# Optimization experiments

Measured on AMD Instinct MI355X. Metric: run time of the kernel, lower is better.

## Reference

```python
import jax, jax.numpy as jnp
import numpy as np

L = 2          # conv layers
N = 50000      # nodes
E = 800000     # edges (before self loops)
F_IN = 256     # raw node features
C = 32         # embed features (out_channels per head)
H = 4          # heads
HC = H * C
ED = 1         # edge feature dim
EPS = 1e-5
NEG_SLOPE = 0.2


def _xavier(k, shape):
    fan_in, fan_out = shape[-2], shape[-1]
    lim = float(np.sqrt(6.0 / (fan_in + fan_out)))
    return jax.random.uniform(k, shape, jnp.float32, -lim, lim)


def setup_inputs() -> dict:
    key = jax.random.key(0)
    ks = jax.random.split(key, 12)
    x = jax.random.normal(ks[0], (N, F_IN), jnp.float32)
    src = jax.random.randint(ks[1], (E,), 0, N, dtype=jnp.int32)
    off = jax.random.randint(ks[2], (E,), 1, N, dtype=jnp.int32)
    dst = (src + off) % N  # guarantees no pre-existing self loops (PyG removes then re-adds them)
    edge_index = jnp.stack([src, dst])
    edge_attr = jax.random.normal(ks[3], (E, ED), jnp.float32)
    return {
        "x": x,
        "edge_index": edge_index,
        "edge_attr": edge_attr,
        "W_emb": _xavier(ks[4], (F_IN, C)),
        "b_emb": jnp.zeros((C,), jnp.float32),
        "ln0_w": jnp.ones((C,), jnp.float32),
        "ln0_b": jnp.zeros((C,), jnp.float32),
        "Wl": _xavier(ks[5], (L, C, HC)),
        "bl": jnp.zeros((L, HC), jnp.float32),
        "Wr": _xavier(ks[6], (L, C, HC)),
        "br": jnp.zeros((L, HC), jnp.float32),
        "We": _xavier(ks[7], (L, ED, HC)),
        "att": jax.random.normal(ks[8], (L, H, C), jnp.float32) * 0.1,
        "gat_b": jnp.zeros((L, HC), jnp.float32),
        "ln1_w": jnp.ones((L, HC), jnp.float32),
        "ln1_b": jnp.zeros((L, HC), jnp.float32),
        "lin_w": _xavier(ks[9], (L, HC, C)),
        "lin_b": jnp.zeros((L, C), jnp.float32),
        "ln2_w": jnp.ones((L, C), jnp.float32),
        "ln2_b": jnp.zeros((L, C), jnp.float32),
    }


def _node_ln(x, w, b):
    # torch.nn.LayerNorm over last dim
    mu = jnp.mean(x, axis=-1, keepdims=True)
    xc = x - mu
    var = jnp.mean(xc * xc, axis=-1, keepdims=True)
    return xc / jnp.sqrt(var + EPS) * w + b


def _graph_ln(x, w, b):
    # torch_geometric.nn.norm.LayerNorm, mode='graph': normalize over ALL nodes+features
    mu = jnp.mean(x)
    xc = x - mu
    var = jnp.mean(xc * xc)
    return xc / jnp.sqrt(var + EPS) * w + b


def _gatv2_layer(h, src, dst, ea, Wl, bl, Wr, br, We, att, gat_b):
    n = h.shape[0]
    xl = (h @ Wl + bl).reshape(n, H, C)   # lin_l(x) -> source transform
    xr = (h @ Wr + br).reshape(n, H, C)   # lin_r(x) -> target transform
    e = (ea @ We).reshape(-1, H, C)       # lin_edge(edge_attr), no bias
    z = jax.nn.leaky_relu(xl[src] + xr[dst] + e, NEG_SLOPE)   # [Etot,H,C]
    logits = jnp.einsum("ehc,hc->eh", z, att)                  # [Etot,H]
    # segment softmax over destination nodes (every node has a self loop)
    m = jax.ops.segment_max(logits, dst, num_segments=n)
    ex = jnp.exp(logits - m[dst])
    s = jax.ops.segment_sum(ex, dst, num_segments=n)
    alpha = ex / s[dst]                                        # [Etot,H]
    msg = alpha[..., None] * xl[src]                           # [Etot,H,C]
    out = jax.ops.segment_sum(msg, dst, num_segments=n)        # [N,H,C]
    return out.reshape(n, HC) + gat_b


def reference(x, edge_index, edge_attr, W_emb, b_emb, ln0_w, ln0_b, Wl, bl, Wr, br,
              We, att, gat_b, ln1_w, ln1_b, lin_w, lin_b, ln2_w, ln2_b):
    n = x.shape[0]
    loop = jnp.arange(n, dtype=edge_index.dtype)
    src = jnp.concatenate([edge_index[0], loop])
    dst = jnp.concatenate([edge_index[1], loop])
    ea = jnp.concatenate([edge_attr, jnp.zeros((n, edge_attr.shape[1]), edge_attr.dtype)])  # fill_value=0.0

    # node_embed: Dropout(eval=identity) -> Linear -> LayerNorm -> ReLU
    h = jax.nn.relu(_node_ln(x @ W_emb + b_emb, ln0_w, ln0_b))
    hs = [h]
    for i in range(L):
        g = _gatv2_layer(h, src, dst, ea, Wl[i], bl[i], Wr[i], br[i], We[i], att[i], gat_b[i])
        g = jax.nn.relu(_graph_ln(g, ln1_w[i], ln1_b[i]))     # PyG graph-mode LayerNorm + ReLU
        g = g @ lin_w[i] + lin_b[i]                            # heads>1 projection back to C
        h = jax.nn.relu(_node_ln(g, ln2_w[i], ln2_b[i]))
        hs.append(h)
    # JumpingKnowledge mode='max': elementwise max over layer outputs
    return jnp.max(jnp.stack(hs, axis=0), axis=0)
```

## Files before the change

### kernel.cpp

```cpp
#include <hip/hip_runtime.h>
#include <hip/hip_fp16.h>

constexpr int kNodes = 50000;
constexpr int kNE    = 800000;
constexpr int kFin   = 256;
constexpr int kC     = 32;
constexpr int kH     = 4;
constexpr int kHC    = 128;
constexpr int kTN    = 16;
constexpr int kWP    = 258;
constexpr int kLWP   = 130;
constexpr int kEmbedBlocks = kNodes / kTN;
constexpr int kHistBlocks  = (kNE + 255) / 256;
constexpr int kTransBlocks = (kNodes + 31) / 32;
constexpr float kEps   = 1e-5f;
constexpr float kSlope = 0.2f;
constexpr float kL2E   = 1.44269504f;
constexpr float kShift2 = 8.0f * 1.44269504f;

template<int CTRL>
__device__ __forceinline__ float dpp_add(float v) {
    int x = __builtin_amdgcn_update_dpp(0, __float_as_int(v), CTRL, 0xF, 0xF, true);
    return v + __int_as_float(x);
}
__device__ __forceinline__ float red16(float p) {
    p = dpp_add<0xB1>(p);
    p = dpp_add<0x4E>(p);
    p = dpp_add<0x141>(p);
    p = dpp_add<0x140>(p);
    return p;
}

__global__ void __launch_bounds__(256) k_fill0(unsigned* __restrict__ p, int n) {
    int i = blockIdx.x * 256 + threadIdx.x;
    if (i < n) p[i] = 0u;
}

__global__ void __launch_bounds__(256) k_embed_hist(
    const float* __restrict__ x, const float* __restrict__ W, const float* __restrict__ b,
    const float* __restrict__ lnw, const float* __restrict__ lnb,
    float* __restrict__ h, float* __restrict__ jk,
    const int* __restrict__ dst, int* __restrict__ deg) {
    __shared__ float sx[kTN * kFin];
    __shared__ float sWt[kC * kWP];
    int t = threadIdx.x;
    if (blockIdx.x >= kEmbedBlocks) {
        int e = (blockIdx.x - kEmbedBlocks) * 256 + t;
        if (e < kNE) atomicAdd(&deg[dst[e]], 1);
        return;
    }
    int n0 = blockIdx.x * kTN;
    for (int i = t; i < kFin * kC; i += 256) {
        int k = i >> 5, c = i & 31;
        sWt[c * kWP + k] = W[i];
    }
    const float* xg = x + (long)n0 * kFin;
    for (int i = t; i < kTN * kFin; i += 256) sx[i] = xg[i];
    __syncthreads();
    int c = t & 31, n2 = t >> 5;
    const float* xa = sx + n2 * kFin;
    const float* xb = sx + (n2 + 8) * kFin;
    const float* wrow = sWt + c * kWP;
    float acc0 = 0.f, acc1 = 0.f;
    #pragma unroll 8
    for (int k = 0; k < kFin; k += 4) {
        float4 x0 = *(const float4*)(xa + k);
        float4 x1 = *(const float4*)(xb + k);
        float2 w0 = *(const float2*)(wrow + k);
        float2 w1 = *(const float2*)(wrow + k + 2);
        acc0 += x0.x * w0.x + x0.y * w0.y + x0.z * w1.x + x0.w * w1.y;
        acc1 += x1.x * w0.x + x1.y * w0.y + x1.z * w1.x + x1.w * w1.y;
    }
    float bc = b[c], lw = lnw[c], lb = lnb[c];
    {
        float y = acc0 + bc;
        float m = y;
        #pragma unroll
        for (int o = 1; o < 32; o <<= 1) m += __shfl_xor(m, o);
        m *= (1.f / kC);
        float xc = y - m, v = xc * xc;
        #pragma unroll
        for (int o = 1; o < 32; o <<= 1) v += __shfl_xor(v, o);
        v *= (1.f / kC);
        float out = fmaxf(xc * rsqrtf(v + kEps) * lw + lb, 0.f);
        int node = n0 + n2;
        h[node * kC + c] = out;
        jk[node * kC + c] = out;
    }
    {
        float y = acc1 + bc;
        float m = y;
        #pragma unroll
        for (int o = 1; o < 32; o <<= 1) m += __shfl_xor(m, o);
        m *= (1.f / kC);
        float xc = y - m, v = xc * xc;
        #pragma unroll
        for (int o = 1; o < 32; o <<= 1) v += __shfl_xor(v, o);
        v *= (1.f / kC);
        float out = fmaxf(xc * rsqrtf(v + kEps) * lw + lb, 0.f);
        int node = n0 + n2 + 8;
        h[node * kC + c] = out;
        jk[node * kC + c] = out;
    }
}

__device__ __forceinline__ void trans_body(
    int bid, float* s_h, const float* __restrict__ h,
    const float* __restrict__ Wl, const float* __restrict__ bl,
    const float* __restrict__ Wr, const float* __restrict__ br,
    __half* __restrict__ xl, float* __restrict__ xr) {
    int t = threadIdx.x;
    int j = t & 127, hf = t >> 7;
    float wl[kC], wr[kC];
    #pragma unroll
    for (int k = 0; k < kC; ++k) { wl[k] = Wl[k * kHC + j]; wr[k] = Wr[k * kHC + j]; }
    float blj = bl[j], brj = br[j];
    int n0 = bid * 32;
    int nn = min(32, kNodes - n0);
    for (int i = t; i < nn * kC; i += 256) s_h[i] = h[n0 * kC + i];
    __syncthreads();
    int nend = min(nn, hf * 16 + 16);
    for (int n = hf * 16; n < nend; ++n) {
        const float4* h4 = (const float4*)(s_h + n * kC);
        float al = blj, ar = brj;
        #pragma unroll
        for (int kq = 0; kq < 8; ++kq) {
            float4 hv = h4[kq];
            al += hv.x * wl[kq*4] + hv.y * wl[kq*4+1] + hv.z * wl[kq*4+2] + hv.w * wl[kq*4+3];
            ar += hv.x * wr[kq*4] + hv.y * wr[kq*4+1] + hv.z * wr[kq*4+2] + hv.w * wr[kq*4+3];
        }
        long g = (long)(n0 + n) * kHC + j;
        xl[g] = __float2half(al);
        xr[g] = ar;
    }
}

__global__ void __launch_bounds__(256) k_trans(
    const float* __restrict__ h,
    const float* __restrict__ Wl, const float* __restrict__ bl,
    const float* __restrict__ Wr, const float* __restrict__ br,
    __half* __restrict__ xl, float* __restrict__ xr) {
    __shared__ float s_h[32 * kC];
    trans_body(blockIdx.x, s_h, h, Wl, bl, Wr, br, xl, xr);
}

__global__ void __launch_bounds__(256) k_trans_reorder(
    const float* __restrict__ h,
    const float* __restrict__ Wl, const float* __restrict__ bl,
    const float* __restrict__ Wr, const float* __restrict__ br,
    __half* __restrict__ xl, float* __restrict__ xr,
    const int* __restrict__ src, const int* __restrict__ dst, const float* __restrict__ ea,
    const int* __restrict__ rowptr, int* __restrict__ cur, int2* __restrict__ epack) {
    __shared__ float s_h[32 * kC];
    if (blockIdx.x < kHistBlocks) {
        int e = blockIdx.x * 256 + threadIdx.x;
        if (e < kNE) {
            int d = dst[e];
            int pos = rowptr[d] + atomicAdd(&cur[d], 1);
            epack[pos] = make_int2(src[e], __float_as_int(ea[e]));
        }
        return;
    }
    trans_body(blockIdx.x - kHistBlocks, s_h, h, Wl, bl, Wr, br, xl, xr);
}

__global__ void __launch_bounds__(256) k_scan1(const int* __restrict__ deg,
                                               int* __restrict__ excl, int* __restrict__ bsum) {
    __shared__ int s[256];
    int t = threadIdx.x;
    int i = blockIdx.x * 256 + t;
    int v = (i < kNodes) ? deg[i] : 0;
    s[t] = v;
    __syncthreads();
    for (int o = 1; o < 256; o <<= 1) {
        int tv = (t >= o) ? s[t - o] : 0;
        __syncthreads();
        s[t] += tv;
        __syncthreads();
    }
    if (i < kNodes) excl[i] = s[t] - v;
    if (t == 255) bsum[blockIdx.x] = s[255];
}

__global__ void __launch_bounds__(256) k_scan2(int* __restrict__ bsum, int nb) {
    __shared__ int s[256];
    int t = threadIdx.x;
    int v = (t < nb) ? bsum[t] : 0;
    s[t] = v;
    __syncthreads();
    for (int o = 1; o < 256; o <<= 1) {
        int tv = (t >= o) ? s[t - o] : 0;
        __syncthreads();
        s[t] += tv;
        __syncthreads();
    }
    if (t < nb) bsum[t] = s[t];
}

__global__ void __launch_bounds__(256) k_scan3(int* __restrict__ excl, const int* __restrict__ bsum) {
    int i = blockIdx.x * 256 + threadIdx.x;
    if (i >= kNodes) return;
    if (blockIdx.x > 0) excl[i] += bsum[blockIdx.x - 1];
}

__global__ void __launch_bounds__(256) k_edge(
    const int* __restrict__ rowptr, const int* __restrict__ deg,
    const int2* __restrict__ epack,
    const __half* __restrict__ xl, float* __restrict__ xrg,
    const float* __restrict__ We, const float* __restrict__ att,
    const float* __restrict__ gat_b, float* __restrict__ ps, float* __restrict__ pq) {
    int t = threadIdx.x & 63;
    int w = __builtin_amdgcn_readfirstlane(threadIdx.x >> 6);
    int d = blockIdx.x * 4 + w;
    const __half2* xl2 = (const __half2*)xl;
    long rowb = (long)d * 64;

    float2 xrv = ((const float2*)xrg)[rowb + t];
    float2 Wev = ((const float2*)We)[t];
    float2 av  = ((const float2*)att)[t];
    av.x *= kL2E; av.y *= kL2E;

    float2 xself = __half22float2(xl2[rowb + t]);

    float z0 = xself.x + xrv.x, z1 = xself.y + xrv.y;
    z0 = fmaxf(z0, kSlope * z0); z1 = fmaxf(z1, kSlope * z1);
    float p = red16(z0 * av.x + z1 * av.y);
    float ee = __builtin_amdgcn_exp2f(p - kShift2);
    float l = ee, o0 = ee * xself.x, o1 = ee * xself.y;

    int base = rowptr[d], cnt = deg[d];
    int e = 0;
    for (; e + 8 <= cnt; e += 8) {
        int se[8]; float ev[8];
        #pragma unroll
        for (int u = 0; u < 8; ++u) {
            int2 ep = epack[base + e + u];
            se[u] = ep.x; ev[u] = __int_as_float(ep.y);
        }
        float2 xv[8]; float pv[8];
        #pragma unroll
        for (int u = 0; u < 8; ++u)
            xv[u] = __half22float2(xl2[(long)se[u] * 64 + t]);
        #pragma unroll
        for (int u = 0; u < 8; ++u) {
            float zz0 = fmaf(ev[u], Wev.x, xrv.x) + xv[u].x;
            float zz1 = fmaf(ev[u], Wev.y, xrv.y) + xv[u].y;
            zz0 = fmaxf(zz0, kSlope * zz0);
            zz1 = fmaxf(zz1, kSlope * zz1);
            pv[u] = red16(zz0 * av.x + zz1 * av.y);
        }
        #pragma unroll
        for (int u = 0; u < 8; ++u) {
            float eeu = __builtin_amdgcn_exp2f(pv[u] - kShift2);
            l += eeu;
            o0 = fmaf(eeu, xv[u].x, o0);
            o1 = fmaf(eeu, xv[u].y, o1);
        }
    }
    for (; e < cnt; ++e) {
        int2 ep = epack[base + e];
        int s = ep.x;
        float eav = __int_as_float(ep.y);
        float2 xv = __half22float2(xl2[(long)s * 64 + t]);
        float zz0 = fmaf(eav, Wev.x, xrv.x) + xv.x;
        float zz1 = fmaf(eav, Wev.y, xrv.y) + xv.y;
        zz0 = fmaxf(zz0, kSlope * zz0);
        zz1 = fmaxf(zz1, kSlope * zz1);
        float pe = red16(zz0 * av.x + zz1 * av.y);
        float eeu = __builtin_amdgcn_exp2f(pe - kShift2);
        l += eeu;
        o0 = fmaf(eeu, xv.x, o0);
        o1 = fmaf(eeu, xv.y, o1);
    }
    float rl = __builtin_amdgcn_rcpf(l);
    float v0 = o0 * rl, v1 = o1 * rl;
    ((float2*)xrg)[rowb + t] = make_float2(v0, v1);
    float2 gb = ((const float2*)gat_b)[t];
    float vb0 = v0 + gb.x, vb1 = v1 + gb.y;
    float s = vb0 + vb1, q = vb0 * vb0 + vb1 * vb1;
    #pragma unroll
    for (int mm = 1; mm < 64; mm <<= 1) { s += __shfl_xor(s, mm); q += __shfl_xor(q, mm); }
    if (t == 0) { ps[d] = s; pq[d] = q; }
}

__global__ void __launch_bounds__(1024) k_statsr(
    const float* __restrict__ ps, const float* __restrict__ pq, float* __restrict__ stats) {
    __shared__ float rs[1024], rq[1024];
    int t = threadIdx.x;
    float s = 0.f, q = 0.f;
    for (int i = t; i < kNodes; i += 1024) { s += ps[i]; q += pq[i]; }
    rs[t] = s; rq[t] = q;
    __syncthreads();
    for (int o = 512; o > 0; o >>= 1) {
        if (t < o) { rs[t] += rs[t + o]; rq[t] += rq[t + o]; }
        __syncthreads();
    }
    if (t == 0) { stats[0] = rs[0]; stats[1] = rq[0]; }
}

__global__ void __launch_bounds__(256) k_post(
    const float* __restrict__ g, const float* __restrict__ gat_b,
    const float* __restrict__ ln1w, const float* __restrict__ ln1b,
    const float* __restrict__ linw, const float* __restrict__ linb,
    const float* __restrict__ ln2w, const float* __restrict__ ln2b,
    const float* __restrict__ stats, const float* __restrict__ jk_in,
    float* __restrict__ h, float* __restrict__ jk_out) {
    __shared__ float s_lwT[kC * kLWP];
    __shared__ float s_vb[8 * kHC];
    int t = threadIdx.x;
    int n0 = blockIdx.x * 8;
    const float inv = 1.f / ((float)kNodes * kHC);
    float mean = stats[0] * inv;
    float var  = stats[1] * inv - mean * mean;
    float rstd = rsqrtf(var + kEps);
    for (int i = t; i < kHC * kC; i += 256) {
        int k = i >> 5, c = i & 31;
        s_lwT[c * kLWP + k] = linw[i];
    }
    for (int i = t; i < 8 * kHC; i += 256) {
        int node = n0 + (i >> 7), f = i & 127;
        float a = (g[(long)node * kHC + f] + gat_b[f] - mean) * rstd * ln1w[f] + ln1b[f];
        s_vb[i] = fmaxf(a, 0.f);
    }
    __syncthreads();
    int n = t >> 5, c = t & 31;
    int node = n0 + n;
    float acc = linb[c];
    const float* vb = s_vb + n * kHC;
    const float* wr = s_lwT + c * kLWP;
    #pragma unroll 8
    for (int k = 0; k < kHC; k += 4) {
        float4 v4 = *(const float4*)(vb + k);
        float2 w0 = *(const float2*)(wr + k);
        float2 w1 = *(const float2*)(wr + k + 2);
        acc += v4.x * w0.x + v4.y * w0.y + v4.z * w1.x + v4.w * w1.y;
    }
    float m = acc;
    #pragma unroll
    for (int mm = 1; mm < 32; mm <<= 1) m += __shfl_xor(m, mm);
    m *= (1.f / kC);
    float dd = acc - m;
    float q = dd * dd;
    #pragma unroll
    for (int mm = 1; mm < 32; mm <<= 1) q += __shfl_xor(q, mm);
    q *= (1.f / kC);
    float out = dd * rsqrtf(q + kEps) * ln2w[c] + ln2b[c];
    out = fmaxf(out, 0.f);
    h[node * kC + c] = out;
    jk_out[node * kC + c] = fmaxf(jk_in[node * kC + c], out);
}

extern "C" void kernel_launch(void* const* d_in, const int* in_sizes, int n_in,
                              void* d_out, int out_size, void* d_ws, size_t ws_size,
                              hipStream_t stream) {
    (void)in_sizes; (void)n_in; (void)out_size; (void)ws_size;
    const float* x     = (const float*)d_in[0];
    const int*   ei    = (const int*)d_in[1];
    const int*   src   = ei;
    const int*   dst   = ei + kNE;
    const float* ea    = (const float*)d_in[2];
    const float* W_emb = (const float*)d_in[3];
    const float* b_emb = (const float*)d_in[4];
    const float* ln0w  = (const float*)d_in[5];
    const float* ln0b  = (const float*)d_in[6];
    const float* Wl    = (const float*)d_in[7];
    const float* bl    = (const float*)d_in[8];
    const float* Wr    = (const float*)d_in[9];
    const float* br    = (const float*)d_in[10];
    const float* We    = (const float*)d_in[11];
    const float* att   = (const float*)d_in[12];
    const float* gat_b = (const float*)d_in[13];
    const float* ln1w  = (const float*)d_in[14];
    const float* ln1b  = (const float*)d_in[15];
    const float* linw  = (const float*)d_in[16];
    const float* linb  = (const float*)d_in[17];
    const float* ln2w  = (const float*)d_in[18];
    const float* ln2b  = (const float*)d_in[19];

    char* wsb = (char*)d_ws;
    float*  h      = (float*)(wsb);
    float*  jk     = (float*)(wsb +  6400000);
    float*  xrg    = (float*)(wsb + 12800000);
    __half* xl     = (__half*)(wsb + 38400000);
    int2*   epack  = (int2*)(wsb + 51200000);
    int*    deg    = (int*)(wsb + 57600000);
    int*    cur    = (int*)(wsb + 57800000);
    int*    rowptr = (int*)(wsb + 58000000);
    int*    bsum   = (int*)(wsb + 58200000);
    float*  stats  = (float*)(wsb + 58201024);
    float*  ps     = (float*)(wsb + 58300000);
    float*  pq     = (float*)(wsb + 58500000);

    const int scanBlocks = (kNodes + 255) / 256;
    const int edgeBlocks = kNodes / 4;
    const int postBlocks = kNodes / 8;

    hipLaunchKernelGGL(k_fill0, dim3((2 * kNodes + 255) / 256), dim3(256), 0, stream,
                       (unsigned*)deg, 2 * kNodes);
    hipLaunchKernelGGL(k_embed_hist, dim3(kEmbedBlocks + kHistBlocks), dim3(256), 0, stream,
                       x, W_emb, b_emb, ln0w, ln0b, h, jk, dst, deg);
    hipLaunchKernelGGL(k_scan1, dim3(scanBlocks), dim3(256), 0, stream, deg, rowptr, bsum);
    hipLaunchKernelGGL(k_scan2, dim3(1), dim3(256), 0, stream, bsum, scanBlocks);
    hipLaunchKernelGGL(k_scan3, dim3(scanBlocks), dim3(256), 0, stream, rowptr, bsum);
    hipLaunchKernelGGL(k_trans_reorder, dim3(kHistBlocks + kTransBlocks), dim3(256), 0, stream,
                       h, Wl, bl, Wr, br, xl, xrg,
                       src, dst, ea, rowptr, cur, epack);
    for (int l = 0; l < 2; ++l) {
        if (l == 1) {
            hipLaunchKernelGGL(k_trans, dim3(kTransBlocks), dim3(256), 0, stream,
                               h, Wl + l * kC * kHC, bl + l * kHC,
                               Wr + l * kC * kHC, br + l * kHC, xl, xrg);
        }
        hipLaunchKernelGGL(k_edge, dim3(edgeBlocks), dim3(256), 0, stream,
                           rowptr, deg, epack, xl, xrg,
                           We + l * kHC, att + l * kH * kC, gat_b + l * kHC, ps, pq);
        hipLaunchKernelGGL(k_statsr, dim3(1), dim3(1024), 0, stream, ps, pq, stats);
        hipLaunchKernelGGL(k_post, dim3(postBlocks), dim3(256), 0, stream,
                           xrg, gat_b + l * kHC, ln1w + l * kHC, ln1b + l * kHC,
                           linw + l * kHC * kC, linb + l * kC,
                           ln2w + l * kC, ln2b + l * kC, stats, jk,
                           h, (l == 1) ? (float*)d_out : jk);
    }
}
```

Before: 463.9 us.

## Process two edges per wavefront in GATv2 edge kernel with half-wave slots

The edge aggregation kernel now splits each 64-lane wavefront into two 32-lane halves. Each half handles alternate edges of the destination node and loads 4 features per lane as an 8-byte half4. The attention dot product uses an 8-lane DPP reduction per head. The two halves' softmax partial sums are merged with a cross-half shuffle at the end. The aim is to double the number of edge gathers in flight per wave and use wider loads. The cost is extra shuffles and more registers per lane.

```diff
diff --git a/kernel.cpp b/kernel.cpp
--- a/kernel.cpp
+++ b/kernel.cpp
@@ -23,11 +23,10 @@
     int x = __builtin_amdgcn_update_dpp(0, __float_as_int(v), CTRL, 0xF, 0xF, true);
     return v + __int_as_float(x);
 }
-__device__ __forceinline__ float red16(float p) {
+__device__ __forceinline__ float red8(float p) {
     p = dpp_add<0xB1>(p);
     p = dpp_add<0x4E>(p);
     p = dpp_add<0x141>(p);
-    p = dpp_add<0x140>(p);
     return p;
 }
 
@@ -209,77 +208,117 @@
     const __half* __restrict__ xl, float* __restrict__ xrg,
     const float* __restrict__ We, const float* __restrict__ att,
     const float* __restrict__ gat_b, float* __restrict__ ps, float* __restrict__ pq) {
+    struct h4 { __half2 a, b; };
     int t = threadIdx.x & 63;
     int w = __builtin_amdgcn_readfirstlane(threadIdx.x >> 6);
     int d = blockIdx.x * 4 + w;
-    const __half2* xl2 = (const __half2*)xl;
-    long rowb = (long)d * 64;
-
-    float2 xrv = ((const float2*)xrg)[rowb + t];
-    float2 Wev = ((const float2*)We)[t];
-    float2 av  = ((const float2*)att)[t];
-    av.x *= kL2E; av.y *= kL2E;
-
-    float2 xself = __half22float2(xl2[rowb + t]);
-
-    float z0 = xself.x + xrv.x, z1 = xself.y + xrv.y;
+    int f = t & 31;
+    bool slot0 = (t < 32);
+    float em0 = slot0 ? 1.f : 0.f;
+
+    const h4* xl4 = (const h4*)xl;
+    long rowq = (long)d * 32;
+
+    float4 xrv = ((const float4*)xrg)[rowq + f];
+    float4 Wev = ((const float4*)We)[f];
+    float4 av  = ((const float4*)att)[f];
+    av.x *= kL2E; av.y *= kL2E; av.z *= kL2E; av.w *= kL2E;
+    float4 gb  = ((const float4*)gat_b)[f];
+
+    h4 xs = xl4[rowq + f];
+    float2 xs01 = __half22float2(xs.a), xs23 = __half22float2(xs.b);
+
+    float z0 = xs01.x + xrv.x, z1 = xs01.y + xrv.y;
+    float z2 = xs23.x + xrv.z, z3 = xs23.y + xrv.w;
     z0 = fmaxf(z0, kSlope * z0); z1 = fmaxf(z1, kSlope * z1);
-    float p = red16(z0 * av.x + z1 * av.y);
-    float ee = __builtin_amdgcn_exp2f(p - kShift2);
-    float l = ee, o0 = ee * xself.x, o1 = ee * xself.y;
+    z2 = fmaxf(z2, kSlope * z2); z3 = fmaxf(z3, kSlope * z3);
+    float p = red8(z0 * av.x + z1 * av.y + z2 * av.z + z3 * av.w);
+    float ee = __builtin_amdgcn_exp2f(p - kShift2) * em0;
+    float l = ee;
+    float o0 = ee * xs01.x, o1 = ee * xs01.y, o2 = ee * xs23.x, o3 = ee * xs23.y;
 
     int base = rowptr[d], cnt = deg[d];
+    int npair = cnt >> 1;
     int e = 0;
-    for (; e + 8 <= cnt; e += 8) {
-        int se[8]; float ev[8];
-        #pragma unroll
-        for (int u = 0; u < 8; ++u) {
-            int2 ep = epack[base + e + u];
-            se[u] = ep.x; ev[u] = __int_as_float(ep.y);
-        }
-        float2 xv[8]; float pv[8];
-        #pragma unroll
-        for (int u = 0; u < 8; ++u)
-            xv[u] = __half22float2(xl2[(long)se[u] * 64 + t]);
-        #pragma unroll
-        for (int u = 0; u < 8; ++u) {
-            float zz0 = fmaf(ev[u], Wev.x, xrv.x) + xv[u].x;
-            float zz1 = fmaf(ev[u], Wev.y, xrv.y) + xv[u].y;
-            zz0 = fmaxf(zz0, kSlope * zz0);
-            zz1 = fmaxf(zz1, kSlope * zz1);
-            pv[u] = red16(zz0 * av.x + zz1 * av.y);
-        }
-        #pragma unroll
-        for (int u = 0; u < 8; ++u) {
-            float eeu = __builtin_amdgcn_exp2f(pv[u] - kShift2);
-            l += eeu;
-            o0 = fmaf(eeu, xv[u].x, o0);
-            o1 = fmaf(eeu, xv[u].y, o1);
-        }
-    }
-    for (; e < cnt; ++e) {
-        int2 ep = epack[base + e];
-        int s = ep.x;
+    for (; e + 4 <= npair; e += 4) {
+        int2 pa[4], pb[4];
+        #pragma unroll
+        for (int u = 0; u < 4; ++u) {
+            pa[u] = epack[base + 2 * (e + u)];
+            pb[u] = epack[base + 2 * (e + u) + 1];
+        }
+        h4 xv[4]; float eav[4];
+        #pragma unroll
+        for (int u = 0; u < 4; ++u) {
+            int srow = slot0 ? pa[u].x : pb[u].x;
+            xv[u] = xl4[(long)srow * 32 + f];
+            eav[u] = __int_as_float(slot0 ? pa[u].y : pb[u].y);
+        }
+        #pragma unroll
+        for (int u = 0; u < 4; ++u) {
+            float2 x01 = __half22float2(xv[u].a), x23 = __half22float2(xv[u].b);
+            float a0 = fmaf(eav[u], Wev.x, xrv.x) + x01.x;
+            float a1 = fmaf(eav[u], Wev.y, xrv.y) + x01.y;
+            float a2 = fmaf(eav[u], Wev.z, xrv.z) + x23.x;
+            float a3 = fmaf(eav[u], Wev.w, xrv.w) + x23.y;
+            a0 = fmaxf(a0, kSlope * a0); a1 = fmaxf(a1, kSlope * a1);
+            a2 = fmaxf(a2, kSlope * a2); a3 = fmaxf(a3, kSlope * a3);
+            float pp = red8(a0 * av.x + a1 * av.y + a2 * av.z + a3 * av.w);
+            float eu = __builtin_amdgcn_exp2f(pp - kShift2);
+            l += eu;
+            o0 = fmaf(eu, x01.x, o0); o1 = fmaf(eu, x01.y, o1);
+            o2 = fmaf(eu, x23.x, o2); o3 = fmaf(eu, x23.y, o3);
+        }
+    }
+    for (; e < npair; ++e) {
+        int2 pa = epack[base + 2 * e];
+        int2 pb = epack[base + 2 * e + 1];
+        int srow = slot0 ? pa.x : pb.x;
+        float eav = __int_as_float(slot0 ? pa.y : pb.y);
+        h4 xv = xl4[(long)srow * 32 + f];
+        float2 x01 = __half22float2(xv.a), x23 = __half22float2(xv.b);
+        float a0 = fmaf(eav, Wev.x, xrv.x) + x01.x;
+        float a1 = fmaf(eav, Wev.y, xrv.y) + x01.y;
+        float a2 = fmaf(eav, Wev.z, xrv.z) + x23.x;
+        float a3 = fmaf(eav, Wev.w, xrv.w) + x23.y;
+        a0 = fmaxf(a0, kSlope * a0); a1 = fmaxf(a1, kSlope * a1);
+        a2 = fmaxf(a2, kSlope * a2); a3 = fmaxf(a3, kSlope * a3);
+        float pp = red8(a0 * av.x + a1 * av.y + a2 * av.z + a3 * av.w);
+        float eu = __builtin_amdgcn_exp2f(pp - kShift2);
+        l += eu;
+        o0 = fmaf(eu, x01.x, o0); o1 = fmaf(eu, x01.y, o1);
+        o2 = fmaf(eu, x23.x, o2); o3 = fmaf(eu, x23.y, o3);
+    }
+    if (cnt & 1) {
+        int2 ep = epack[base + cnt - 1];
+        int srow = ep.x;
         float eav = __int_as_float(ep.y);
-        float2 xv = __half22float2(xl2[(long)s * 64 + t]);
-        float zz0 = fmaf(eav, Wev.x, xrv.x) + xv.x;
-        float zz1 = fmaf(eav, Wev.y, xrv.y) + xv.y;
-        zz0 = fmaxf(zz0, kSlope * zz0);
-        zz1 = fmaxf(zz1, kSlope * zz1);
-        float pe = red16(zz0 * av.x + zz1 * av.y);
-        float eeu = __builtin_amdgcn_exp2f(pe - kShift2);
-        l += eeu;
-        o0 = fmaf(eeu, xv.x, o0);
-        o1 = fmaf(eeu, xv.y, o1);
-    }
+        h4 xv = xl4[(long)srow * 32 + f];
+        float2 x01 = __half22float2(xv.a), x23 = __half22float2(xv.b);
+        float a0 = fmaf(eav, Wev.x, xrv.x) + x01.x;
+        float a1 = fmaf(eav, Wev.y, xrv.y) + x01.y;
+        float a2 = fmaf(eav, Wev.z, xrv.z) + x23.x;
+        float a3 = fmaf(eav, Wev.w, xrv.w) + x23.y;
+        a0 = fmaxf(a0, kSlope * a0); a1 = fmaxf(a1, kSlope * a1);
+        a2 = fmaxf(a2, kSlope * a2); a3 = fmaxf(a3, kSlope * a3);
+        float pp = red8(a0 * av.x + a1 * av.y + a2 * av.z + a3 * av.w);
+        float eu = __builtin_amdgcn_exp2f(pp - kShift2) * em0;
+        l += eu;
+        o0 = fmaf(eu, x01.x, o0); o1 = fmaf(eu, x01.y, o1);
+        o2 = fmaf(eu, x23.x, o2); o3 = fmaf(eu, x23.y, o3);
+    }
+    l  += __shfl_xor(l, 32);
+    o0 += __shfl_xor(o0, 32); o1 += __shfl_xor(o1, 32);
+    o2 += __shfl_xor(o2, 32); o3 += __shfl_xor(o3, 32);
     float rl = __builtin_amdgcn_rcpf(l);
-    float v0 = o0 * rl, v1 = o1 * rl;
-    ((float2*)xrg)[rowb + t] = make_float2(v0, v1);
-    float2 gb = ((const float2*)gat_b)[t];
-    float vb0 = v0 + gb.x, vb1 = v1 + gb.y;
-    float s = vb0 + vb1, q = vb0 * vb0 + vb1 * vb1;
+    float v0 = o0 * rl, v1 = o1 * rl, v2 = o2 * rl, v3 = o3 * rl;
+    if (slot0)
+        ((float4*)xrg)[rowq + f] = make_float4(v0, v1, v2, v3);
+    float vb0 = v0 + gb.x, vb1 = v1 + gb.y, vb2 = v2 + gb.z, vb3 = v3 + gb.w;
+    float s = vb0 + vb1 + vb2 + vb3;
+    float q = vb0 * vb0 + vb1 * vb1 + vb2 * vb2 + vb3 * vb3;
     #pragma unroll
-    for (int mm = 1; mm < 64; mm <<= 1) { s += __shfl_xor(s, mm); q += __shfl_xor(q, mm); }
+    for (int mm = 1; mm < 32; mm <<= 1) { s += __shfl_xor(s, mm); q += __shfl_xor(q, mm); }
     if (t == 0) { ps[d] = s; pq[d] = q; }
 }
 
```

New measurement: 462.6 us. About the same (-0.3%).
